# Kernel tuning notes

Hardware: AMD Instinct MI355X
Metric: run time of the kernel (lower is better)

Reference implementation:

```python
import jax, jax.numpy as jnp
import numpy as np

N = 50000
E = 800000
D = 64


def setup_inputs() -> dict:
    key = jax.random.key(0)
    k1, k2, k3, k4, k5, k6 = jax.random.split(key, 6)
    node_feats = jax.random.normal(k1, (N, D), dtype=jnp.float32)
    edge_feats = jax.random.normal(k2, (E, D), dtype=jnp.float32)
    src = jax.random.randint(k3, (E,), 0, N, dtype=jnp.int32)
    dst = jnp.sort(jax.random.randint(k4, (E,), 0, N, dtype=jnp.int32))
    # Linear(in_feats=D, out_feats=D) parameters (PyTorch default init scale)
    lim = 1.0 / np.sqrt(D)
    W = jax.random.uniform(k5, (D, D), minval=-lim, maxval=lim, dtype=jnp.float32)
    b = jax.random.uniform(k6, (D,), minval=-lim, maxval=lim, dtype=jnp.float32)
    return {"node_feats": node_feats, "edge_feats": edge_feats, "src": src,
            "dst": dst, "W": W, "b": b}


def reference(node_feats, edge_feats, src, dst, W, b):
    # u_add_e: per-edge message m_e = h_src(e) + h_e   [E, D]
    m = node_feats[src] + edge_feats
    # edge_softmax over edges grouped by destination node, per feature dim
    seg_max = jax.ops.segment_max(m, dst, num_segments=N)        # [N, D]
    seg_max = jnp.where(jnp.isfinite(seg_max), seg_max, 0.0)     # nodes w/o in-edges
    ex = jnp.exp(m - seg_max[dst])                               # [E, D]
    denom = jax.ops.segment_sum(ex, dst, num_segments=N)         # [N, D]
    a = ex / jnp.maximum(denom[dst], 1e-38)                      # [E, D]
    # weighted scatter-sum: h'_v = sum_{e->v} m_e * a_e
    agg = jax.ops.segment_sum(m * a, dst, num_segments=N)        # [N, D]
    # MLP + activation + residual (dropout=0, output_norm='none')
    out = jax.nn.relu(agg @ W.T + b) + node_feats
    return out
```

## Files before the change

### kernel.cpp

```cpp
#include <hip/hip_runtime.h>
#include <math.h>

#define DD 64
typedef float v4f __attribute__((ext_vector_type(4)));

__global__ void prep_kernel(const int* __restrict__ dst,
                            const float* __restrict__ W,
                            int* __restrict__ row_start,
                            float* __restrict__ WT,
                            int N, int E) {
    int t = blockIdx.x * blockDim.x + threadIdx.x;
    if (t < DD * DD) {
        int j = t / DD;
        int d = t % DD;
        WT[d * DD + j] = W[t];
    }
    if (t <= N) {
        if (t == N) {
            row_start[N] = E;
        } else {
            int lo = 0, hi = E;
            while (lo < hi) {
                int mid = (lo + hi) >> 1;
                if (dst[mid] < t) lo = mid + 1; else hi = mid;
            }
            row_start[t] = lo;
        }
    }
}

__global__ __launch_bounds__(256) void gcn_main(
    const float* __restrict__ node_feats,
    const float* __restrict__ edge_feats,
    const int*   __restrict__ src,
    const float* __restrict__ bvec,
    const int*   __restrict__ row_start,
    const float* __restrict__ WT,
    float*       __restrict__ out,
    int N)
{
    const int wave = threadIdx.x >> 6;
    const int lane = threadIdx.x & 63;
    const int grp  = lane >> 4;
    const int qd   = lane & 15;
    const int v = blockIdx.x * 4 + wave;
    if (v >= N) return;

    const int e0 = row_start[v];
    const int e1 = row_start[v + 1];

    const v4f* __restrict__ nf4 = (const v4f*)node_feats;
    const v4f* __restrict__ ef4 = (const v4f*)edge_feats;

    v4f se = {0.f, 0.f, 0.f, 0.f};
    v4f sm = {0.f, 0.f, 0.f, 0.f};

    for (int eb = e0; eb < e1; eb += 8) {
        const int ea  = eb + grp;
        const int eb2 = eb + 4 + grp;
        const bool va = ea  < e1;
        const bool vb = eb2 < e1;
        const int eca = va ? ea  : e0;
        const int ecb = vb ? eb2 : e0;
        const int sa = src[eca];
        const int sb = src[ecb];
        const v4f ga = __builtin_nontemporal_load(ef4 + (size_t)eca * 16 + qd);
        const v4f gb = __builtin_nontemporal_load(ef4 + (size_t)ecb * 16 + qd);
        const v4f na = nf4[(size_t)sa * 16 + qd];
        const v4f nb = nf4[(size_t)sb * 16 + qd];
        const v4f ma = na + ga;
        const v4f mb = nb + gb;
        v4f xa, xb;
        xa.x = va ? __expf(ma.x) : 0.f;
        xa.y = va ? __expf(ma.y) : 0.f;
        xa.z = va ? __expf(ma.z) : 0.f;
        xa.w = va ? __expf(ma.w) : 0.f;
        xb.x = vb ? __expf(mb.x) : 0.f;
        xb.y = vb ? __expf(mb.y) : 0.f;
        xb.z = vb ? __expf(mb.z) : 0.f;
        xb.w = vb ? __expf(mb.w) : 0.f;
        se += xa;  se += xb;
        sm += ma * xa;  sm += mb * xb;
    }

    for (int off = 16; off < 64; off <<= 1) {
        se.x += __shfl_xor(se.x, off, 64);
        se.y += __shfl_xor(se.y, off, 64);
        se.z += __shfl_xor(se.z, off, 64);
        se.w += __shfl_xor(se.w, off, 64);
        sm.x += __shfl_xor(sm.x, off, 64);
        sm.y += __shfl_xor(sm.y, off, 64);
        sm.z += __shfl_xor(sm.z, off, 64);
        sm.w += __shfl_xor(sm.w, off, 64);
    }

    float agarr[4];
    agarr[0] = sm.x / fmaxf(se.x, 1e-38f);
    agarr[1] = sm.y / fmaxf(se.y, 1e-38f);
    agarr[2] = sm.z / fmaxf(se.z, 1e-38f);
    agarr[3] = sm.w / fmaxf(se.w, 1e-38f);

    const v4f* __restrict__ WT4 = (const v4f*)WT;
    v4f acc = {0.f, 0.f, 0.f, 0.f};
#pragma unroll
    for (int k = 0; k < 16; ++k) {
        const float ad = __shfl(agarr[k & 3], grp * 4 + (k >> 2), 64);
        const v4f w = WT4[(size_t)(grp * 16 + k) * 16 + qd];
        acc.x = fmaf(ad, w.x, acc.x);
        acc.y = fmaf(ad, w.y, acc.y);
        acc.z = fmaf(ad, w.z, acc.z);
        acc.w = fmaf(ad, w.w, acc.w);
    }
    for (int off = 16; off < 64; off <<= 1) {
        acc.x += __shfl_xor(acc.x, off, 64);
        acc.y += __shfl_xor(acc.y, off, 64);
        acc.z += __shfl_xor(acc.z, off, 64);
        acc.w += __shfl_xor(acc.w, off, 64);
    }
    if (grp == 0) {
        const v4f bb = ((const v4f*)bvec)[qd];
        const v4f nv = nf4[(size_t)v * 16 + qd];
        v4f o;
        o.x = fmaxf(acc.x + bb.x, 0.f) + nv.x;
        o.y = fmaxf(acc.y + bb.y, 0.f) + nv.y;
        o.z = fmaxf(acc.z + bb.z, 0.f) + nv.z;
        o.w = fmaxf(acc.w + bb.w, 0.f) + nv.w;
        ((v4f*)out)[(size_t)v * 16 + qd] = o;
    }
}

extern "C" void kernel_launch(void* const* d_in, const int* in_sizes, int n_in,
                              void* d_out, int out_size, void* d_ws, size_t ws_size,
                              hipStream_t stream) {
    const float* node_feats = (const float*)d_in[0];
    const float* edge_feats = (const float*)d_in[1];
    const int*   src        = (const int*)  d_in[2];
    const int*   dst        = (const int*)  d_in[3];
    const float* W          = (const float*)d_in[4];
    const float* bvec       = (const float*)d_in[5];
    float*       out        = (float*)d_out;

    const int N = in_sizes[0] / DD;
    const int E = in_sizes[2];

    int*   row_start = (int*)d_ws;
    size_t wt_off = (((size_t)(N + 1) * sizeof(int)) + 255) & ~(size_t)255;
    float* WT = (float*)((char*)d_ws + wt_off);

    {
        int total = (N + 1) > DD * DD ? (N + 1) : DD * DD;
        int blocks = (total + 255) / 256;
        prep_kernel<<<blocks, 256, 0, stream>>>(dst, W, row_start, WT, N, E);
    }
    {
        int blocks = (N + 3) / 4;
        gcn_main<<<blocks, 256, 0, stream>>>(node_feats, edge_feats, src, bvec,
                                             row_start, WT, out, N);
    }
}
```

Before: 329.0 us.

## Split node MLP out of aggregation kernel into separate register-tiled kernel

The fused aggregation+MLP kernel becomes two kernels. The aggregation kernel writes the softmax-weighted sum for each node to a workspace buffer. A new MLP kernel holds one row of W per lane in registers and streams 16 nodes per wave, broadcasting each agg row. This drops the per-node W reload and shuffle-based matvec from the gather-bound kernel, but adds a kernel launch plus a write and re-read of a 50000x64 intermediate.

```diff
diff --git a/kernel.cpp b/kernel.cpp
--- a/kernel.cpp
+++ b/kernel.cpp
@@ -5,16 +5,9 @@
 typedef float v4f __attribute__((ext_vector_type(4)));
 
 __global__ void prep_kernel(const int* __restrict__ dst,
-                            const float* __restrict__ W,
                             int* __restrict__ row_start,
-                            float* __restrict__ WT,
                             int N, int E) {
     int t = blockIdx.x * blockDim.x + threadIdx.x;
-    if (t < DD * DD) {
-        int j = t / DD;
-        int d = t % DD;
-        WT[d * DD + j] = W[t];
-    }
     if (t <= N) {
         if (t == N) {
             row_start[N] = E;
@@ -29,14 +22,12 @@
     }
 }
 
-__global__ __launch_bounds__(256) void gcn_main(
+__global__ __launch_bounds__(256) void agg_kernel(
     const float* __restrict__ node_feats,
     const float* __restrict__ edge_feats,
     const int*   __restrict__ src,
-    const float* __restrict__ bvec,
     const int*   __restrict__ row_start,
-    const float* __restrict__ WT,
-    float*       __restrict__ out,
+    float*       __restrict__ agg,
     int N)
 {
     const int wave = threadIdx.x >> 6;
@@ -94,38 +85,50 @@
         sm.w += __shfl_xor(sm.w, off, 64);
     }
 
-    float agarr[4];
-    agarr[0] = sm.x / fmaxf(se.x, 1e-38f);
-    agarr[1] = sm.y / fmaxf(se.y, 1e-38f);
-    agarr[2] = sm.z / fmaxf(se.z, 1e-38f);
-    agarr[3] = sm.w / fmaxf(se.w, 1e-38f);
+    if (grp == 0) {
+        v4f a;
+        a.x = sm.x / fmaxf(se.x, 1e-38f);
+        a.y = sm.y / fmaxf(se.y, 1e-38f);
+        a.z = sm.z / fmaxf(se.z, 1e-38f);
+        a.w = sm.w / fmaxf(se.w, 1e-38f);
+        ((v4f*)agg)[(size_t)v * 16 + qd] = a;
+    }
+}
 
-    const v4f* __restrict__ WT4 = (const v4f*)WT;
-    v4f acc = {0.f, 0.f, 0.f, 0.f};
+__global__ __launch_bounds__(256) void mlp_kernel(
+    const float* __restrict__ agg,
+    const float* __restrict__ node_feats,
+    const float* __restrict__ W,
+    const float* __restrict__ bvec,
+    float*       __restrict__ out,
+    int N)
+{
+    const int lane = threadIdx.x & 63;
+    const int wave = threadIdx.x >> 6;
+
+    v4f wreg[16];
 #pragma unroll
-    for (int k = 0; k < 16; ++k) {
-        const float ad = __shfl(agarr[k & 3], grp * 4 + (k >> 2), 64);
-        const v4f w = WT4[(size_t)(grp * 16 + k) * 16 + qd];
-        acc.x = fmaf(ad, w.x, acc.x);
-        acc.y = fmaf(ad, w.y, acc.y);
-        acc.z = fmaf(ad, w.z, acc.z);
-        acc.w = fmaf(ad, w.w, acc.w);
-    }
-    for (int off = 16; off < 64; off <<= 1) {
-        acc.x += __shfl_xor(acc.x, off, 64);
-        acc.y += __shfl_xor(acc.y, off, 64);
-        acc.z += __shfl_xor(acc.z, off, 64);
-        acc.w += __shfl_xor(acc.w, off, 64);
-    }
-    if (grp == 0) {
-        const v4f bb = ((const v4f*)bvec)[qd];
-        const v4f nv = nf4[(size_t)v * 16 + qd];
-        v4f o;
-        o.x = fmaxf(acc.x + bb.x, 0.f) + nv.x;
-        o.y = fmaxf(acc.y + bb.y, 0.f) + nv.y;
-        o.z = fmaxf(acc.z + bb.z, 0.f) + nv.z;
-        o.w = fmaxf(acc.w + bb.w, 0.f) + nv.w;
-        ((v4f*)out)[(size_t)v * 16 + qd] = o;
+    for (int q = 0; q < 16; ++q)
+        wreg[q] = ((const v4f*)W)[(size_t)lane * 16 + q];
+    const float bj = bvec[lane];
+
+    const int v0    = blockIdx.x * 64 + wave * 16;
+    const int v_end = (v0 + 16 < N) ? (v0 + 16) : N;
+
+    for (int v = v0; v < v_end; ++v) {
+        const int vu = __builtin_amdgcn_readfirstlane(v);
+        const v4f* __restrict__ arow = (const v4f*)(agg + (size_t)vu * DD);
+        float acc = bj;
+#pragma unroll
+        for (int q = 0; q < 16; ++q) {
+            const v4f a = arow[q];
+            acc = fmaf(a.x, wreg[q].x, acc);
+            acc = fmaf(a.y, wreg[q].y, acc);
+            acc = fmaf(a.z, wreg[q].z, acc);
+            acc = fmaf(a.w, wreg[q].w, acc);
+        }
+        const float res = node_feats[(size_t)vu * DD + lane];
+        out[(size_t)vu * DD + lane] = fmaxf(acc, 0.f) + res;
     }
 }
 
@@ -144,17 +147,20 @@
     const int E = in_sizes[2];
 
     int*   row_start = (int*)d_ws;
-    size_t wt_off = (((size_t)(N + 1) * sizeof(int)) + 255) & ~(size_t)255;
-    float* WT = (float*)((char*)d_ws + wt_off);
+    size_t agg_off = (((size_t)(N + 1) * sizeof(int)) + 255) & ~(size_t)255;
+    float* agg = (float*)((char*)d_ws + agg_off);
 
     {
-        int total = (N + 1) > DD * DD ? (N + 1) : DD * DD;
-        int blocks = (total + 255) / 256;
-        prep_kernel<<<blocks, 256, 0, stream>>>(dst, W, row_start, WT, N, E);
+        int blocks = (N + 1 + 255) / 256;
+        prep_kernel<<<blocks, 256, 0, stream>>>(dst, row_start, N, E);
     }
     {
         int blocks = (N + 3) / 4;
-        gcn_main<<<blocks, 256, 0, stream>>>(node_feats, edge_feats, src, bvec,
-                                             row_start, WT, out, N);
+        agg_kernel<<<blocks, 256, 0, stream>>>(node_feats, edge_feats, src,
+                                               row_start, agg, N);
+    }
+    {
+        int blocks = (N + 63) / 64;
+        mlp_kernel<<<blocks, 256, 0, stream>>>(agg, node_feats, W, bvec, out, N);
     }
 }
```

Measured after the change: 325.3 us. Within noise of the previous version (-1.1%).
